# Kernel tuning notes

Measured on AMD Instinct MI355X. Metric: run time of the kernel, lower is better.

## Reference

```python
import jax, jax.numpy as jnp
import numpy as np

B, T, D = 8, 4096, 512
EXPAND = 2
DI = D * EXPAND          # d_inner = 1024
K = 7                    # d_conv
LN_EPS = 1e-5


def setup_inputs() -> dict:
    key = jax.random.key(0)
    ks = jax.random.split(key, 12)
    s = 0.02
    return {
        "x": jax.random.normal(ks[0], (B, T, D), dtype=jnp.float32),
        # shared input projection (no bias): weight (2*DI, D), torch Linear layout
        "in_proj_w": jax.random.normal(ks[1], (2 * DI, D), dtype=jnp.float32) * s,
        # forward Conv1DSequenceMixer: depthwise conv (DI,1,K) + bias, proj Linear (DI,DI)+bias
        "conv_fwd_w": jax.random.normal(ks[2], (DI, 1, K), dtype=jnp.float32) * s,
        "conv_fwd_b": jnp.zeros((DI,), dtype=jnp.float32),
        "proj_fwd_w": jax.random.normal(ks[3], (DI, DI), dtype=jnp.float32) * s,
        "proj_fwd_b": jnp.zeros((DI,), dtype=jnp.float32),
        # backward Conv1DSequenceMixer
        "conv_bwd_w": jax.random.normal(ks[4], (DI, 1, K), dtype=jnp.float32) * s,
        "conv_bwd_b": jnp.zeros((DI,), dtype=jnp.float32),
        "proj_bwd_w": jax.random.normal(ks[5], (DI, DI), dtype=jnp.float32) * s,
        "proj_bwd_b": jnp.zeros((DI,), dtype=jnp.float32),
        # diagonal term and gate scale
        "diag_weight": jnp.full((DI,), 0.1, dtype=jnp.float32),
        "gate_scale": jnp.full((1,), 0.5, dtype=jnp.float32),
        # output projection (no bias): (D, DI)
        "out_proj_w": jax.random.normal(ks[6], (D, DI), dtype=jnp.float32) * s,
        # LayerNorm
        "ln_g": jnp.ones((D,), dtype=jnp.float32),
        "ln_b": jnp.zeros((D,), dtype=jnp.float32),
    }


def _seq_mixer(x, conv_w, conv_b, proj_w, proj_b):
    """Conv1DSequenceMixer: causal depthwise conv + SiLU(Linear). x: (B,T,C)."""
    C = x.shape[-1]
    # torch pads both sides by K-1 then truncates to T -> equivalent to causal left-pad
    xp = jnp.pad(x, ((0, 0), (K - 1, 0), (0, 0)))            # (B, T+K-1, C)
    y = jax.lax.conv_general_dilated(
        xp.transpose(0, 2, 1), conv_w, window_strides=(1,), padding="VALID",
        dimension_numbers=("NCH", "OIH", "NCH"), feature_group_count=C,
    )                                                         # (B, C, T)
    y = y.transpose(0, 2, 1) + conv_b                         # (B, T, C)
    y = jnp.einsum("btc,oc->bto", y, proj_w) + proj_b
    return jax.nn.silu(y)


def _shift_right(x):
    """Shift one step right along time, zero-padding the first step."""
    return jnp.pad(x, ((0, 0), (1, 0), (0, 0)))[:, :-1, :]


def reference(x, in_proj_w, conv_fwd_w, conv_fwd_b, proj_fwd_w, proj_fwd_b,
              conv_bwd_w, conv_bwd_b, proj_bwd_w, proj_bwd_b,
              diag_weight, gate_scale, out_proj_w, ln_g, ln_b):
    residual = x
    xz = jnp.einsum("btd,ed->bte", x, in_proj_w)              # (B,T,2*DI)
    x_proj, z = xz[..., :DI], xz[..., DI:]

    y_fwd = _shift_right(_seq_mixer(x_proj, conv_fwd_w, conv_fwd_b, proj_fwd_w, proj_fwd_b))

    x_flip = jnp.flip(x_proj, axis=1)
    y_bwd = _shift_right(_seq_mixer(x_flip, conv_bwd_w, conv_bwd_b, proj_bwd_w, proj_bwd_b))
    y_bwd = jnp.flip(y_bwd, axis=1)

    y = y_fwd + y_bwd + x_proj * diag_weight                  # quasiseparable sum
    y = y * jax.nn.silu(z) * gate_scale                       # SiLU gate + scale
    y = jnp.einsum("bte,de->btd", y, out_proj_w)              # out_proj (no bias)

    h = residual + y                                          # dropout=0 (eval)
    mu = jnp.mean(h, axis=-1, keepdims=True)
    var = jnp.var(h, axis=-1, keepdims=True)
    return (h - mu) * jax.lax.rsqrt(var + LN_EPS) * ln_g + ln_b
```

## Files before the change

### kernel.cpp

```cpp
#include <hip/hip_runtime.h>
#include <hip/hip_bf16.h>
#include <cstdint>

#define T_SEQ  4096
#define DMODEL 512
#define DINNER 1024
#define MTOT   32768

typedef __bf16 bf16_t;
typedef bf16_t bf16x8 __attribute__((ext_vector_type(8)));
typedef bf16_t bf16x4v __attribute__((ext_vector_type(4)));
typedef float  f32x4  __attribute__((ext_vector_type(4)));

__device__ __forceinline__ void async_copy16(const bf16_t* g, bf16_t* l) {
  __builtin_amdgcn_global_load_lds(
      (const __attribute__((address_space(1))) void*)g,
      (__attribute__((address_space(3))) void*)l,
      16, 0, 0);
}

__device__ __forceinline__ float silu_f(float v) {
  return v / (1.f + __expf(-v));
}

__global__ __launch_bounds__(256) void cast_kernel(
    const float* __restrict__ s, bf16_t* __restrict__ d, int n4)
{
  const int i = blockIdx.x * 256 + threadIdx.x;
  if (i < n4) {
    const f32x4 v = ((const f32x4*)s)[i];
    bf16x4v o;
    o[0] = (bf16_t)v[0]; o[1] = (bf16_t)v[1];
    o[2] = (bf16_t)v[2]; o[3] = (bf16_t)v[3];
    ((bf16x4v*)d)[i] = o;
  }
}

__global__ __launch_bounds__(256) void wtr_kernel(
    const float* __restrict__ w, float* __restrict__ wt)
{
  const int i = blockIdx.x * 256 + threadIdx.x;
  if (i < 7 * DINNER) {
    const int c = i & (DINNER - 1);
    const int k = i >> 10;
    wt[i] = w[c * 7 + k];
  }
}

template <int EPI>
__global__ __launch_bounds__(256, 2) void gemm_bt(
    const bf16_t* __restrict__ A, const bf16_t* __restrict__ B,
    bf16_t* __restrict__ Cb, float* __restrict__ Cf,
    const float* __restrict__ bias, const float* __restrict__ resid,
    int N, int K)
{
  constexpr int BM = 128, BN = 128, BK = 64;
  __shared__ __attribute__((aligned(16))) bf16_t sA[BM * BK];
  __shared__ __attribute__((aligned(16))) bf16_t sB[BN * BK];

  const int tid  = threadIdx.x;

  int bflat;
  {
    const int nwg = gridDim.x * gridDim.y;
    const int orig = blockIdx.y * gridDim.x + blockIdx.x;
    const int q = nwg >> 3, r = nwg & 7;
    const int xcd = orig & 7, lid = orig >> 3;
    bflat = (xcd < r ? xcd * (q + 1) : r * (q + 1) + (xcd - r) * q) + lid;
  }
  const int m0 = (bflat / gridDim.x) * BM;
  const int n0 = (bflat % gridDim.x) * BN;

  const int w    = tid >> 6, lane = tid & 63;
  const int wm   = (w & 1) << 6, wn = (w >> 1) << 6;
  const int quad = lane >> 4, lrow = lane & 15;

  f32x4 acc[4][4] = {};

  for (int kt = 0; kt < K; kt += BK) {
    __syncthreads();
#pragma unroll
    for (int i = 0; i < 4; ++i) {
      const int f = (i * 256 + tid) << 3;
      const int r = f >> 6, c = f & 63;
      async_copy16(&A[(size_t)(m0 + r) * K + kt + c], &sA[f]);
      async_copy16(&B[(size_t)(n0 + r) * K + kt + c], &sB[f]);
    }
    __syncthreads();
#pragma unroll
    for (int ks = 0; ks < 2; ++ks) {
      bf16x8 av[4], bv[4];
#pragma unroll
      for (int i = 0; i < 4; ++i) {
        av[i] = *(const bf16x8*)&sA[(wm + i * 16 + lrow) * BK + ks * 32 + (quad << 3)];
        bv[i] = *(const bf16x8*)&sB[(wn + i * 16 + lrow) * BK + ks * 32 + (quad << 3)];
      }
#pragma unroll
      for (int mi = 0; mi < 4; ++mi)
#pragma unroll
        for (int ni = 0; ni < 4; ++ni)
          acc[mi][ni] = __builtin_amdgcn_mfma_f32_16x16x32_bf16(
              av[mi], bv[ni], acc[mi][ni], 0, 0, 0);
    }
  }

#pragma unroll
  for (int mi = 0; mi < 4; ++mi)
#pragma unroll
    for (int ni = 0; ni < 4; ++ni)
#pragma unroll
      for (int r = 0; r < 4; ++r) {
        const int row = m0 + wm + mi * 16 + (quad << 2) + r;
        const int col = n0 + wn + ni * 16 + lrow;
        float v = acc[mi][ni][r];
        if constexpr (EPI == 0) {
          Cb[(size_t)row * N + col] = (bf16_t)v;
        } else if constexpr (EPI == 1) {
          v += bias[col];
          Cb[(size_t)row * N + col] = (bf16_t)silu_f(v);
        } else {
          v += resid[(size_t)row * N + col];
          Cf[(size_t)row * N + col] = v;
        }
      }
}

template <int DIR>
__global__ __launch_bounds__(256) void conv_kernel(
    const bf16_t* __restrict__ xzc,
    const float* __restrict__ wt, const float* __restrict__ bc,
    bf16_t* __restrict__ vout, int r0, int loc0, int Mc)
{
  const int idx = blockIdx.x * 256 + threadIdx.x;
  const int c8  = idx & 127;
  const int tg  = idx >> 7;
  const int bt0 = tg << 2;
  const int t0  = (bt0 + r0) & (T_SEQ - 1);
  const int lt0 = bt0 + loc0;
  const int cc  = c8 << 3;

  float wv[7][8];
#pragma unroll
  for (int k = 0; k < 7; ++k) {
    const f32x4 a = *(const f32x4*)&wt[k * DINNER + cc];
    const f32x4 b = *(const f32x4*)&wt[k * DINNER + cc + 4];
#pragma unroll
    for (int u = 0; u < 4; ++u) { wv[k][u] = a[u]; wv[k][u + 4] = b[u]; }
  }

  float acc[4][8];
  {
    const f32x4 a = *(const f32x4*)&bc[cc];
    const f32x4 b = *(const f32x4*)&bc[cc + 4];
#pragma unroll
    for (int i = 0; i < 4; ++i)
#pragma unroll
      for (int u = 0; u < 4; ++u) { acc[i][u] = a[u]; acc[i][u + 4] = b[u]; }
  }

#pragma unroll
  for (int rr = 0; rr < 10; ++rr) {
    int lt = (DIR == 0) ? (lt0 - 7 + rr) : (lt0 + 1 + rr);
    lt = lt < 0 ? 0 : (lt > Mc - 1 ? Mc - 1 : lt);
    const bf16x8 xv = *(const bf16x8*)&xzc[(size_t)lt * 2048 + cc];
    float xf[8];
#pragma unroll
    for (int u = 0; u < 8; ++u) xf[u] = (float)xv[u];
#pragma unroll
    for (int i = 0; i < 4; ++i) {
      const int k = (DIR == 0) ? (rr - i) : (i + 6 - rr);
      if (k >= 0 && k <= 6) {
        const bool ok = (DIR == 0) ? (t0 + i >= 7 - k)
                                   : (t0 + i <= (T_SEQ - 8) + k);
        if (ok) {
#pragma unroll
          for (int u = 0; u < 8; ++u) acc[i][u] += wv[k][u] * xf[u];
        }
      }
    }
  }

#pragma unroll
  for (int i = 0; i < 4; ++i) {
    bf16x8 o;
#pragma unroll
    for (int u = 0; u < 8; ++u) o[u] = (bf16_t)acc[i][u];
    *(bf16x8*)&vout[(size_t)(bt0 + i) * DINNER + cc] = o;
  }
}

__global__ __launch_bounds__(256) void gate_kernel(
    const bf16_t* __restrict__ xzc,
    const bf16_t* __restrict__ sf, bf16_t* __restrict__ sb_g,
    const float* __restrict__ diag, const float* __restrict__ gs,
    int r0, int loc0)
{
  const int idx = blockIdx.x * 256 + threadIdx.x;
  const int e8  = idx & 127;
  const int btl = idx >> 7;
  const int t   = (btl + r0) & (T_SEQ - 1);
  const int lt  = btl + loc0;
  const int ee  = e8 << 3;

  const bf16x8 xp  = *(const bf16x8*)&xzc[(size_t)lt * 2048 + ee];
  const bf16x8 zz  = *(const bf16x8*)&xzc[(size_t)lt * 2048 + DINNER + ee];
  const bf16x8 sfv = *(const bf16x8*)&sf[(size_t)btl * DINNER + ee];
  const bf16x8 sbv = *(const bf16x8*)&sb_g[(size_t)btl * DINNER + ee];
  const f32x4 d0 = *(const f32x4*)&diag[ee];
  const f32x4 d1 = *(const f32x4*)&diag[ee + 4];
  const float g = gs[0];
  const bool addf = (t > 0), addb = (t < T_SEQ - 1);

  bf16x8 o;
#pragma unroll
  for (int u = 0; u < 8; ++u) {
    float y = (float)xp[u] * (u < 4 ? d0[u] : d1[u - 4]);
    if (addf) y += (float)sfv[u];
    if (addb) y += (float)sbv[u];
    o[u] = (bf16_t)(y * silu_f((float)zz[u]) * g);
  }
  *(bf16x8*)&sb_g[(size_t)btl * DINNER + ee] = o;
}

__global__ __launch_bounds__(256) void ln_kernel(
    const float* __restrict__ h,
    const float* __restrict__ lng, const float* __restrict__ lnb,
    float* __restrict__ out, int r0)
{
  const int row = blockIdx.x;
  const int tid = threadIdx.x;
  const float* hr = h + (size_t)row * DMODEL;
  const float v0 = hr[tid], v1 = hr[tid + 256];
  float s  = v0 + v1;
  float ss = v0 * v0 + v1 * v1;
#pragma unroll
  for (int off = 1; off < 64; off <<= 1) {
    s  += __shfl_xor(s, off);
    ss += __shfl_xor(ss, off);
  }
  __shared__ float ps[8];
  const int w = tid >> 6;
  if ((tid & 63) == 0) { ps[w] = s; ps[w + 4] = ss; }
  __syncthreads();
  s  = ps[0] + ps[1] + ps[2] + ps[3];
  ss = ps[4] + ps[5] + ps[6] + ps[7];
  const float mu  = s * (1.f / DMODEL);
  const float inv = rsqrtf(ss * (1.f / DMODEL) - mu * mu + 1e-5f);
  float* o = out + (size_t)(r0 + row) * DMODEL;
  o[tid]       = (v0 - mu) * inv * lng[tid]       + lnb[tid];
  o[tid + 256] = (v1 - mu) * inv * lng[tid + 256] + lnb[tid + 256];
}

extern "C" void kernel_launch(void* const* d_in, const int* in_sizes, int n_in,
                              void* d_out, int out_size, void* d_ws, size_t ws_size,
                              hipStream_t stream) {
  const float* x    = (const float*)d_in[0];
  const float* in_w = (const float*)d_in[1];
  const float* cfw  = (const float*)d_in[2];
  const float* cfb  = (const float*)d_in[3];
  const float* pfw  = (const float*)d_in[4];
  const float* pfb  = (const float*)d_in[5];
  const float* cbw  = (const float*)d_in[6];
  const float* cbb  = (const float*)d_in[7];
  const float* pbw  = (const float*)d_in[8];
  const float* pbb  = (const float*)d_in[9];
  const float* diag = (const float*)d_in[10];
  const float* gs   = (const float*)d_in[11];
  const float* ow   = (const float*)d_in[12];
  const float* lng  = (const float*)d_in[13];
  const float* lnb  = (const float*)d_in[14];
  float* out = (float*)d_out;

  char* ws = (char*)d_ws;

  bf16_t* xw   = (bf16_t*)(ws);
  bf16_t* inwb = (bf16_t*)(ws + (size_t)33554432);
  bf16_t* pfwb = (bf16_t*)(ws + (size_t)35651584);
  bf16_t* pbwb = (bf16_t*)(ws + (size_t)37748736);
  bf16_t* owb  = (bf16_t*)(ws + (size_t)39845888);
  float*  wtf  = (float*)(ws + (size_t)40894464);
  float*  wtb  = (float*)(ws + (size_t)40923136);
  const size_t persist = 40951808;

  int CH = 128;
  {
    const int cands[8] = {16384, 8192, 4096, 2048, 1024, 512, 256, 128};
    for (int i = 0; i < 8; ++i) {
      const size_t req = persist + (size_t)(cands[i] + 256) * 4096 +
                         (size_t)3 * cands[i] * 2048;
      if (ws_size >= req) { CH = cands[i]; break; }
    }
  }

  char* cb = ws + persist;
  const size_t xz_cap = (size_t)(CH + 256) * 4096;
  bf16_t* xzc  = (bf16_t*)cb;
  bf16_t* bufA = (bf16_t*)(cb + xz_cap);
  bf16_t* bufB = (bf16_t*)(cb + xz_cap + (size_t)CH * 2048);
  bf16_t* bufC = (bf16_t*)(cb + xz_cap + (size_t)CH * 4096);
  float*  hbuf = (float*)cb;

  dim3 blk(256);

  cast_kernel<<<dim3(16384), blk, 0, stream>>>(x,    xw,   4194304);
  cast_kernel<<<dim3(1024),  blk, 0, stream>>>(in_w, inwb, 262144);
  cast_kernel<<<dim3(1024),  blk, 0, stream>>>(pfw,  pfwb, 262144);
  cast_kernel<<<dim3(1024),  blk, 0, stream>>>(pbw,  pbwb, 262144);
  cast_kernel<<<dim3(512),   blk, 0, stream>>>(ow,   owb,  131072);
  wtr_kernel<<<dim3(28), blk, 0, stream>>>(cfw, wtf);
  wtr_kernel<<<dim3(28), blk, 0, stream>>>(cbw, wtb);

  for (int r0 = 0; r0 < MTOT; r0 += CH) {
    const int g0 = (r0 >= 128) ? (r0 - 128) : 0;
    int g1 = r0 + CH + 128; if (g1 > MTOT) g1 = MTOT;
    const int Mc   = g1 - g0;
    const int loc0 = r0 - g0;

    gemm_bt<0><<<dim3(2048 / 128, Mc / 128), blk, 0, stream>>>(
        xw + (size_t)g0 * 512, inwb, xzc, nullptr, nullptr, nullptr, 2048, 512);

    conv_kernel<0><<<dim3(CH / 8), blk, 0, stream>>>(
        xzc, wtf, cfb, bufA, r0, loc0, Mc);

    gemm_bt<1><<<dim3(1024 / 128, CH / 128), blk, 0, stream>>>(
        bufA, pfwb, bufB, nullptr, pfb, nullptr, 1024, 1024);

    conv_kernel<1><<<dim3(CH / 8), blk, 0, stream>>>(
        xzc, wtb, cbb, bufA, r0, loc0, Mc);

    gemm_bt<1><<<dim3(1024 / 128, CH / 128), blk, 0, stream>>>(
        bufA, pbwb, bufC, nullptr, pbb, nullptr, 1024, 1024);

    gate_kernel<<<dim3(CH / 2), blk, 0, stream>>>(
        xzc, bufB, bufC, diag, gs, r0, loc0);

    gemm_bt<2><<<dim3(512 / 128, CH / 128), blk, 0, stream>>>(
        bufC, owb, nullptr, hbuf, nullptr, x + (size_t)r0 * 512, 512, 1024);

    ln_kernel<<<dim3(CH), blk, 0, stream>>>(hbuf, lng, lnb, out, r0);
  }
}
```

Before: 680.1 us.

## Fuse forward/backward projection GEMMs with gating epilogue into one dual GEMM

Replaces the two separate projection GEMMs (bias+SiLU epilogue) and the standalone gate kernel with a single kernel that computes both products per tile and applies the diag, SiLU gate and scale in its epilogue. This drops the round trip of the two intermediate bf16 activations through global memory and two kernel launches per chunk. The dual kernel doubles accumulators and LDS (64KB), which lowers occupancy. The remaining gemm_bt launch bound is raised to 3 waves per SIMD, and its epilogue reads xzc element-wise with uncoalesced scalar loads.

```diff
diff --git a/kernel.cpp b/kernel.cpp
--- a/kernel.cpp
+++ b/kernel.cpp
@@ -21,6 +21,14 @@
 
 __device__ __forceinline__ float silu_f(float v) {
   return v / (1.f + __expf(-v));
+}
+
+__device__ __forceinline__ int xcd_swizzle_flat() {
+  const int nwg = gridDim.x * gridDim.y;
+  const int orig = blockIdx.y * gridDim.x + blockIdx.x;
+  const int q = nwg >> 3, r = nwg & 7;
+  const int xcd = orig & 7, lid = orig >> 3;
+  return (xcd < r ? xcd * (q + 1) : r * (q + 1) + (xcd - r) * q) + lid;
 }
 
 __global__ __launch_bounds__(256) void cast_kernel(
@@ -48,10 +56,10 @@
 }
 
 template <int EPI>
-__global__ __launch_bounds__(256, 2) void gemm_bt(
+__global__ __launch_bounds__(256, 3) void gemm_bt(
     const bf16_t* __restrict__ A, const bf16_t* __restrict__ B,
     bf16_t* __restrict__ Cb, float* __restrict__ Cf,
-    const float* __restrict__ bias, const float* __restrict__ resid,
+    const float* __restrict__ resid,
     int N, int K)
 {
   constexpr int BM = 128, BN = 128, BK = 64;
@@ -59,15 +67,7 @@
   __shared__ __attribute__((aligned(16))) bf16_t sB[BN * BK];
 
   const int tid  = threadIdx.x;
-
-  int bflat;
-  {
-    const int nwg = gridDim.x * gridDim.y;
-    const int orig = blockIdx.y * gridDim.x + blockIdx.x;
-    const int q = nwg >> 3, r = nwg & 7;
-    const int xcd = orig & 7, lid = orig >> 3;
-    bflat = (xcd < r ? xcd * (q + 1) : r * (q + 1) + (xcd - r) * q) + lid;
-  }
+  const int bflat = xcd_swizzle_flat();
   const int m0 = (bflat / gridDim.x) * BM;
   const int n0 = (bflat % gridDim.x) * BN;
 
@@ -115,14 +115,113 @@
         float v = acc[mi][ni][r];
         if constexpr (EPI == 0) {
           Cb[(size_t)row * N + col] = (bf16_t)v;
-        } else if constexpr (EPI == 1) {
-          v += bias[col];
-          Cb[(size_t)row * N + col] = (bf16_t)silu_f(v);
         } else {
           v += resid[(size_t)row * N + col];
           Cf[(size_t)row * N + col] = v;
         }
       }
+}
+
+__global__ __launch_bounds__(256, 2) void gemm_dual(
+    const bf16_t* __restrict__ A1, const bf16_t* __restrict__ A2,
+    const bf16_t* __restrict__ B1, const bf16_t* __restrict__ B2,
+    const float* __restrict__ b1, const float* __restrict__ b2,
+    const bf16_t* __restrict__ xzc, const float* __restrict__ diag,
+    const float* __restrict__ gs, bf16_t* __restrict__ G,
+    int r0, int loc0, int N, int K)
+{
+  constexpr int BM = 128, BN = 128, BK = 64;
+  __shared__ __attribute__((aligned(16))) bf16_t sA1[BM * BK];
+  __shared__ __attribute__((aligned(16))) bf16_t sA2[BM * BK];
+  __shared__ __attribute__((aligned(16))) bf16_t sB1[BN * BK];
+  __shared__ __attribute__((aligned(16))) bf16_t sB2[BN * BK];
+
+  const int tid  = threadIdx.x;
+  const int bflat = xcd_swizzle_flat();
+  const int m0 = (bflat / gridDim.x) * BM;
+  const int n0 = (bflat % gridDim.x) * BN;
+
+  const int w    = tid >> 6, lane = tid & 63;
+  const int wm   = (w & 1) << 6, wn = (w >> 1) << 6;
+  const int quad = lane >> 4, lrow = lane & 15;
+
+  f32x4 accf[4][4] = {};
+  f32x4 accb[4][4] = {};
+
+  for (int kt = 0; kt < K; kt += BK) {
+    __syncthreads();
+#pragma unroll
+    for (int i = 0; i < 4; ++i) {
+      const int f = (i * 256 + tid) << 3;
+      const int r = f >> 6, c = f & 63;
+      const size_t ga = (size_t)(m0 + r) * K + kt + c;
+      const size_t gb = (size_t)(n0 + r) * K + kt + c;
+      async_copy16(&A1[ga], &sA1[f]);
+      async_copy16(&A2[ga], &sA2[f]);
+      async_copy16(&B1[gb], &sB1[f]);
+      async_copy16(&B2[gb], &sB2[f]);
+    }
+    __syncthreads();
+#pragma unroll
+    for (int ks = 0; ks < 2; ++ks) {
+      const int ko = ks * 32 + (quad << 3);
+      bf16x8 av[4], bv[4];
+#pragma unroll
+      for (int i = 0; i < 4; ++i) {
+        av[i] = *(const bf16x8*)&sA1[(wm + i * 16 + lrow) * BK + ko];
+        bv[i] = *(const bf16x8*)&sB1[(wn + i * 16 + lrow) * BK + ko];
+      }
+#pragma unroll
+      for (int mi = 0; mi < 4; ++mi)
+#pragma unroll
+        for (int ni = 0; ni < 4; ++ni)
+          accf[mi][ni] = __builtin_amdgcn_mfma_f32_16x16x32_bf16(
+              av[mi], bv[ni], accf[mi][ni], 0, 0, 0);
+#pragma unroll
+      for (int i = 0; i < 4; ++i) {
+        av[i] = *(const bf16x8*)&sA2[(wm + i * 16 + lrow) * BK + ko];
+        bv[i] = *(const bf16x8*)&sB2[(wn + i * 16 + lrow) * BK + ko];
+      }
+#pragma unroll
+      for (int mi = 0; mi < 4; ++mi)
+#pragma unroll
+        for (int ni = 0; ni < 4; ++ni)
+          accb[mi][ni] = __builtin_amdgcn_mfma_f32_16x16x32_bf16(
+              av[mi], bv[ni], accb[mi][ni], 0, 0, 0);
+    }
+  }
+
+  const float gsv = gs[0];
+  int   colv[4];
+  float b1v[4], b2v[4], dgv[4];
+#pragma unroll
+  for (int ni = 0; ni < 4; ++ni) {
+    const int col = n0 + wn + ni * 16 + lrow;
+    colv[ni] = col;
+    b1v[ni] = b1[col];
+    b2v[ni] = b2[col];
+    dgv[ni] = diag[col];
+  }
+#pragma unroll
+  for (int mi = 0; mi < 4; ++mi)
+#pragma unroll
+    for (int r = 0; r < 4; ++r) {
+      const int row = m0 + wm + mi * 16 + (quad << 2) + r;
+      const int t = (row + r0) & (T_SEQ - 1);
+      const bool tf = (t > 0), tb = (t < T_SEQ - 1);
+      const bf16_t* xrow = &xzc[(size_t)(loc0 + row) * 2048];
+#pragma unroll
+      for (int ni = 0; ni < 4; ++ni) {
+        const float sf = silu_f(accf[mi][ni][r] + b1v[ni]);
+        const float sb = silu_f(accb[mi][ni][r] + b2v[ni]);
+        const float xp = (float)xrow[colv[ni]];
+        const float z  = (float)xrow[colv[ni] + DINNER];
+        float y = xp * dgv[ni];
+        if (tf) y += sf;
+        if (tb) y += sb;
+        G[(size_t)row * N + colv[ni]] = (bf16_t)(y * silu_f(z) * gsv);
+      }
+    }
 }
 
 template <int DIR>
@@ -187,39 +286,6 @@
     for (int u = 0; u < 8; ++u) o[u] = (bf16_t)acc[i][u];
     *(bf16x8*)&vout[(size_t)(bt0 + i) * DINNER + cc] = o;
   }
-}
-
-__global__ __launch_bounds__(256) void gate_kernel(
-    const bf16_t* __restrict__ xzc,
-    const bf16_t* __restrict__ sf, bf16_t* __restrict__ sb_g,
-    const float* __restrict__ diag, const float* __restrict__ gs,
-    int r0, int loc0)
-{
-  const int idx = blockIdx.x * 256 + threadIdx.x;
-  const int e8  = idx & 127;
-  const int btl = idx >> 7;
-  const int t   = (btl + r0) & (T_SEQ - 1);
-  const int lt  = btl + loc0;
-  const int ee  = e8 << 3;
-
-  const bf16x8 xp  = *(const bf16x8*)&xzc[(size_t)lt * 2048 + ee];
-  const bf16x8 zz  = *(const bf16x8*)&xzc[(size_t)lt * 2048 + DINNER + ee];
-  const bf16x8 sfv = *(const bf16x8*)&sf[(size_t)btl * DINNER + ee];
-  const bf16x8 sbv = *(const bf16x8*)&sb_g[(size_t)btl * DINNER + ee];
-  const f32x4 d0 = *(const f32x4*)&diag[ee];
-  const f32x4 d1 = *(const f32x4*)&diag[ee + 4];
-  const float g = gs[0];
-  const bool addf = (t > 0), addb = (t < T_SEQ - 1);
-
-  bf16x8 o;
-#pragma unroll
-  for (int u = 0; u < 8; ++u) {
-    float y = (float)xp[u] * (u < 4 ? d0[u] : d1[u - 4]);
-    if (addf) y += (float)sfv[u];
-    if (addb) y += (float)sbv[u];
-    o[u] = (bf16_t)(y * silu_f((float)zz[u]) * g);
-  }
-  *(bf16x8*)&sb_g[(size_t)btl * DINNER + ee] = o;
 }
 
 __global__ __launch_bounds__(256) void ln_kernel(
@@ -317,25 +383,20 @@
     const int loc0 = r0 - g0;
 
     gemm_bt<0><<<dim3(2048 / 128, Mc / 128), blk, 0, stream>>>(
-        xw + (size_t)g0 * 512, inwb, xzc, nullptr, nullptr, nullptr, 2048, 512);
+        xw + (size_t)g0 * 512, inwb, xzc, nullptr, nullptr, 2048, 512);
 
     conv_kernel<0><<<dim3(CH / 8), blk, 0, stream>>>(
         xzc, wtf, cfb, bufA, r0, loc0, Mc);
 
-    gemm_bt<1><<<dim3(1024 / 128, CH / 128), blk, 0, stream>>>(
-        bufA, pfwb, bufB, nullptr, pfb, nullptr, 1024, 1024);
-
     conv_kernel<1><<<dim3(CH / 8), blk, 0, stream>>>(
-        xzc, wtb, cbb, bufA, r0, loc0, Mc);
-
-    gemm_bt<1><<<dim3(1024 / 128, CH / 128), blk, 0, stream>>>(
-        bufA, pbwb, bufC, nullptr, pbb, nullptr, 1024, 1024);
-
-    gate_kernel<<<dim3(CH / 2), blk, 0, stream>>>(
-        xzc, bufB, bufC, diag, gs, r0, loc0);
+        xzc, wtb, cbb, bufB, r0, loc0, Mc);
+
+    gemm_dual<<<dim3(1024 / 128, CH / 128), blk, 0, stream>>>(
+        bufA, bufB, pfwb, pbwb, pfb, pbb, xzc, diag, gs, bufC,
+        r0, loc0, 1024, 1024);
 
     gemm_bt<2><<<dim3(512 / 128, CH / 128), blk, 0, stream>>>(
-        bufC, owb, nullptr, hbuf, nullptr, x + (size_t)r0 * 512, 512, 1024);
+        bufC, owb, nullptr, hbuf, x + (size_t)r0 * 512, 512, 1024);
 
     ln_kernel<<<dim3(CH), blk, 0, stream>>>(hbuf, lng, lnb, out, r0);
   }
```

Result: faster. 647.3 us (-4.8%).

## Double-buffer GEMM LDS tiles and fuse gate into backward proj GEMM epilogue

Applied to the files above, without the earlier changes.

The GEMM now keeps two LDS buffers so the async global-to-LDS load of the next K tile is issued before computing the current one, with a single barrier per iteration. The separate gate kernel is removed and its work (diag term, forward/backward sum with boundary masks, SiLU(z) gate and scale) moves into a new epilogue of the backward projection GEMM, which saves one full read/write pass over an intermediate buffer and a kernel launch. Bias and diag loads are hoisted out of the epilogue loop. Doubling LDS to 64KB per block may reduce occupancy, and the fused epilogue does scalar, poorly coalesced reads of xzc and the forward result.

```diff
diff --git a/kernel.cpp b/kernel.cpp
--- a/kernel.cpp
+++ b/kernel.cpp
@@ -21,6 +21,14 @@
 
 __device__ __forceinline__ float silu_f(float v) {
   return v / (1.f + __expf(-v));
+}
+
+__device__ __forceinline__ int xcd_swizzle_flat() {
+  const int nwg = gridDim.x * gridDim.y;
+  const int orig = blockIdx.y * gridDim.x + blockIdx.x;
+  const int q = nwg >> 3, r = nwg & 7;
+  const int xcd = orig & 7, lid = orig >> 3;
+  return (xcd < r ? xcd * (q + 1) : r * (q + 1) + (xcd - r) * q) + lid;
 }
 
 __global__ __launch_bounds__(256) void cast_kernel(
@@ -52,22 +60,16 @@
     const bf16_t* __restrict__ A, const bf16_t* __restrict__ B,
     bf16_t* __restrict__ Cb, float* __restrict__ Cf,
     const float* __restrict__ bias, const float* __restrict__ resid,
-    int N, int K)
+    const bf16_t* __restrict__ sf, const bf16_t* __restrict__ xzc,
+    const float* __restrict__ diag, const float* __restrict__ gs,
+    int r0, int loc0, int N, int K)
 {
   constexpr int BM = 128, BN = 128, BK = 64;
-  __shared__ __attribute__((aligned(16))) bf16_t sA[BM * BK];
-  __shared__ __attribute__((aligned(16))) bf16_t sB[BN * BK];
+  __shared__ __attribute__((aligned(16))) bf16_t sA[2][BM * BK];
+  __shared__ __attribute__((aligned(16))) bf16_t sB[2][BN * BK];
 
   const int tid  = threadIdx.x;
-
-  int bflat;
-  {
-    const int nwg = gridDim.x * gridDim.y;
-    const int orig = blockIdx.y * gridDim.x + blockIdx.x;
-    const int q = nwg >> 3, r = nwg & 7;
-    const int xcd = orig & 7, lid = orig >> 3;
-    bflat = (xcd < r ? xcd * (q + 1) : r * (q + 1) + (xcd - r) * q) + lid;
-  }
+  const int bflat = xcd_swizzle_flat();
   const int m0 = (bflat / gridDim.x) * BM;
   const int n0 = (bflat % gridDim.x) * BN;
 
@@ -77,23 +79,30 @@
 
   f32x4 acc[4][4] = {};
 
-  for (int kt = 0; kt < K; kt += BK) {
-    __syncthreads();
+  auto STAGE = [&](int kt, int bb) {
 #pragma unroll
     for (int i = 0; i < 4; ++i) {
       const int f = (i * 256 + tid) << 3;
       const int r = f >> 6, c = f & 63;
-      async_copy16(&A[(size_t)(m0 + r) * K + kt + c], &sA[f]);
-      async_copy16(&B[(size_t)(n0 + r) * K + kt + c], &sB[f]);
-    }
-    __syncthreads();
+      async_copy16(&A[(size_t)(m0 + r) * K + kt + c], &sA[bb][f]);
+      async_copy16(&B[(size_t)(n0 + r) * K + kt + c], &sB[bb][f]);
+    }
+  };
+
+  STAGE(0, 0);
+  __syncthreads();
+
+  int cur = 0;
+  for (int kt = 0; kt < K; kt += BK) {
+    if (kt + BK < K) STAGE(kt + BK, cur ^ 1);
 #pragma unroll
     for (int ks = 0; ks < 2; ++ks) {
+      const int ko = ks * 32 + (quad << 3);
       bf16x8 av[4], bv[4];
 #pragma unroll
       for (int i = 0; i < 4; ++i) {
-        av[i] = *(const bf16x8*)&sA[(wm + i * 16 + lrow) * BK + ks * 32 + (quad << 3)];
-        bv[i] = *(const bf16x8*)&sB[(wn + i * 16 + lrow) * BK + ks * 32 + (quad << 3)];
+        av[i] = *(const bf16x8*)&sA[cur][(wm + i * 16 + lrow) * BK + ko];
+        bv[i] = *(const bf16x8*)&sB[cur][(wn + i * 16 + lrow) * BK + ko];
       }
 #pragma unroll
       for (int mi = 0; mi < 4; ++mi)
@@ -102,27 +111,57 @@
           acc[mi][ni] = __builtin_amdgcn_mfma_f32_16x16x32_bf16(
               av[mi], bv[ni], acc[mi][ni], 0, 0, 0);
     }
-  }
+    __syncthreads();
+    cur ^= 1;
+  }
+
+  float b1v[4], dgv[4];
+  if constexpr (EPI == 1 || EPI == 3) {
+#pragma unroll
+    for (int ni = 0; ni < 4; ++ni) b1v[ni] = bias[n0 + wn + ni * 16 + lrow];
+  }
+  if constexpr (EPI == 3) {
+#pragma unroll
+    for (int ni = 0; ni < 4; ++ni) dgv[ni] = diag[n0 + wn + ni * 16 + lrow];
+  }
+  const float gsv = (EPI == 3) ? gs[0] : 0.f;
 
 #pragma unroll
   for (int mi = 0; mi < 4; ++mi)
 #pragma unroll
-    for (int ni = 0; ni < 4; ++ni)
-#pragma unroll
-      for (int r = 0; r < 4; ++r) {
-        const int row = m0 + wm + mi * 16 + (quad << 2) + r;
-        const int col = n0 + wn + ni * 16 + lrow;
-        float v = acc[mi][ni][r];
-        if constexpr (EPI == 0) {
-          Cb[(size_t)row * N + col] = (bf16_t)v;
-        } else if constexpr (EPI == 1) {
-          v += bias[col];
-          Cb[(size_t)row * N + col] = (bf16_t)silu_f(v);
-        } else {
-          v += resid[(size_t)row * N + col];
-          Cf[(size_t)row * N + col] = v;
+    for (int r = 0; r < 4; ++r) {
+      const int row = m0 + wm + mi * 16 + (quad << 2) + r;
+      if constexpr (EPI == 3) {
+        const int t = (row + r0) & (T_SEQ - 1);
+        const bool tf = (t > 0), tb = (t < T_SEQ - 1);
+        const bf16_t* xrow = &xzc[(size_t)(loc0 + row) * 2048];
+#pragma unroll
+        for (int ni = 0; ni < 4; ++ni) {
+          const int col = n0 + wn + ni * 16 + lrow;
+          const float sb = silu_f(acc[mi][ni][r] + b1v[ni]);
+          const float xp = (float)xrow[col];
+          const float z  = (float)xrow[col + DINNER];
+          float y = xp * dgv[ni];
+          if (tf) y += (float)sf[(size_t)row * N + col];
+          if (tb) y += sb;
+          Cb[(size_t)row * N + col] = (bf16_t)(y * silu_f(z) * gsv);
+        }
+      } else {
+#pragma unroll
+        for (int ni = 0; ni < 4; ++ni) {
+          const int col = n0 + wn + ni * 16 + lrow;
+          float v = acc[mi][ni][r];
+          if constexpr (EPI == 0) {
+            Cb[(size_t)row * N + col] = (bf16_t)v;
+          } else if constexpr (EPI == 1) {
+            Cb[(size_t)row * N + col] = (bf16_t)silu_f(v + b1v[ni]);
+          } else {
+            v += resid[(size_t)row * N + col];
+            Cf[(size_t)row * N + col] = v;
+          }
         }
       }
+    }
 }
 
 template <int DIR>
@@ -187,39 +226,6 @@
     for (int u = 0; u < 8; ++u) o[u] = (bf16_t)acc[i][u];
     *(bf16x8*)&vout[(size_t)(bt0 + i) * DINNER + cc] = o;
   }
-}
-
-__global__ __launch_bounds__(256) void gate_kernel(
-    const bf16_t* __restrict__ xzc,
-    const bf16_t* __restrict__ sf, bf16_t* __restrict__ sb_g,
-    const float* __restrict__ diag, const float* __restrict__ gs,
-    int r0, int loc0)
-{
-  const int idx = blockIdx.x * 256 + threadIdx.x;
-  const int e8  = idx & 127;
-  const int btl = idx >> 7;
-  const int t   = (btl + r0) & (T_SEQ - 1);
-  const int lt  = btl + loc0;
-  const int ee  = e8 << 3;
-
-  const bf16x8 xp  = *(const bf16x8*)&xzc[(size_t)lt * 2048 + ee];
-  const bf16x8 zz  = *(const bf16x8*)&xzc[(size_t)lt * 2048 + DINNER + ee];
-  const bf16x8 sfv = *(const bf16x8*)&sf[(size_t)btl * DINNER + ee];
-  const bf16x8 sbv = *(const bf16x8*)&sb_g[(size_t)btl * DINNER + ee];
-  const f32x4 d0 = *(const f32x4*)&diag[ee];
-  const f32x4 d1 = *(const f32x4*)&diag[ee + 4];
-  const float g = gs[0];
-  const bool addf = (t > 0), addb = (t < T_SEQ - 1);
-
-  bf16x8 o;
-#pragma unroll
-  for (int u = 0; u < 8; ++u) {
-    float y = (float)xp[u] * (u < 4 ? d0[u] : d1[u - 4]);
-    if (addf) y += (float)sfv[u];
-    if (addb) y += (float)sbv[u];
-    o[u] = (bf16_t)(y * silu_f((float)zz[u]) * g);
-  }
-  *(bf16x8*)&sb_g[(size_t)btl * DINNER + ee] = o;
 }
 
 __global__ __launch_bounds__(256) void ln_kernel(
@@ -317,25 +323,26 @@
     const int loc0 = r0 - g0;
 
     gemm_bt<0><<<dim3(2048 / 128, Mc / 128), blk, 0, stream>>>(
-        xw + (size_t)g0 * 512, inwb, xzc, nullptr, nullptr, nullptr, 2048, 512);
+        xw + (size_t)g0 * 512, inwb, xzc, nullptr, nullptr, nullptr,
+        nullptr, nullptr, nullptr, nullptr, 0, 0, 2048, 512);
 
     conv_kernel<0><<<dim3(CH / 8), blk, 0, stream>>>(
         xzc, wtf, cfb, bufA, r0, loc0, Mc);
 
+    conv_kernel<1><<<dim3(CH / 8), blk, 0, stream>>>(
+        xzc, wtb, cbb, bufB, r0, loc0, Mc);
+
     gemm_bt<1><<<dim3(1024 / 128, CH / 128), blk, 0, stream>>>(
-        bufA, pfwb, bufB, nullptr, pfb, nullptr, 1024, 1024);
-
-    conv_kernel<1><<<dim3(CH / 8), blk, 0, stream>>>(
-        xzc, wtb, cbb, bufA, r0, loc0, Mc);
-
-    gemm_bt<1><<<dim3(1024 / 128, CH / 128), blk, 0, stream>>>(
-        bufA, pbwb, bufC, nullptr, pbb, nullptr, 1024, 1024);
-
-    gate_kernel<<<dim3(CH / 2), blk, 0, stream>>>(
-        xzc, bufB, bufC, diag, gs, r0, loc0);
+        bufA, pfwb, bufC, nullptr, pfb, nullptr,
+        nullptr, nullptr, nullptr, nullptr, 0, 0, 1024, 1024);
+
+    gemm_bt<3><<<dim3(1024 / 128, CH / 128), blk, 0, stream>>>(
+        bufB, pbwb, bufA, nullptr, pbb, nullptr,
+        bufC, xzc, diag, gs, r0, loc0, 1024, 1024);
 
     gemm_bt<2><<<dim3(512 / 128, CH / 128), blk, 0, stream>>>(
-        bufC, owb, nullptr, hbuf, nullptr, x + (size_t)r0 * 512, 512, 1024);
+        bufA, owb, nullptr, hbuf, nullptr, x + (size_t)r0 * 512,
+        nullptr, nullptr, nullptr, nullptr, 0, 0, 512, 1024);
 
     ln_kernel<<<dim3(CH), blk, 0, stream>>>(hbuf, lng, lnb, out, r0);
   }
```

New measurement: 786.9 us. +15.7%, slower.
